# Performance work log

Hardware: AMD Instinct MI355X
Metric: run time of the kernel (lower is better)

The kernel has to match this reference:

```python
import jax, jax.numpy as jnp
import numpy as np

B, C, H, W = 64, 3, 224, 224
PH = PW = 16
GH, GW = H // PH, W // PW
NP = GH * GW                        # 196 patches
E = 512                             # embed_dim == decoder_dim
NH = 8                              # num_heads
PPD = C * PH * PW                   # 768 pixels per patch
MASK_RATIO = 0.75
NUM_MASKED = int(MASK_RATIO * NP)   # 147


def setup_inputs() -> dict:
    key = jax.random.key(0)
    ks = jax.random.split(key, 16)
    s = 0.02
    x = jax.random.normal(ks[0], (B, C, H, W), jnp.float32)
    # per-sample random permutation (torch.rand().argsort() equivalent)
    shuffle_indices = jax.vmap(lambda k: jax.random.permutation(k, NP))(
        jax.random.split(ks[1], B)).astype(jnp.int32)
    return {
        "x": x,
        "shuffle_indices": shuffle_indices,
        "W_pe": jax.random.normal(ks[2], (E, PPD), jnp.float32) * s,
        "b_pe": jnp.zeros((E,), jnp.float32),
        "pos_embed": jax.random.normal(ks[3], (1, NP, E), jnp.float32),
        "enc_W": jax.random.normal(ks[4], (E, E), jnp.float32) * s,
        "enc_b": jnp.zeros((E,), jnp.float32),
        "in_proj_w": jax.random.normal(ks[5], (3 * E, E), jnp.float32) * s,
        "in_proj_b": jnp.zeros((3 * E,), jnp.float32),
        "out_w": jax.random.normal(ks[6], (E, E), jnp.float32) * s,
        "out_b": jnp.zeros((E,), jnp.float32),
        "head_W": jax.random.normal(ks[7], (PPD, E), jnp.float32) * s,
        "head_b": jnp.zeros((PPD,), jnp.float32),
        # torch.randn_like(mask_patches) noise, passed in for determinism
        "noise": jax.random.normal(ks[8], (B, NUM_MASKED, PPD), jnp.float32),
    }


def _to_img(p):
    # [b, nP, ph*pw*c] -> [b, c, H, W] (inverse of patchify)
    return p.reshape(B, GH, GW, PH, PW, C).transpose(0, 5, 1, 3, 2, 4).reshape(B, C, H, W)


def reference(x, shuffle_indices, W_pe, b_pe, pos_embed, enc_W, enc_b,
              in_proj_w, in_proj_b, out_w, out_b, head_W, head_b, noise):
    hd = E // NH
    # patchify: [b,c,H,W] -> [b, nP, ph*pw*c]
    patches = x.reshape(B, C, GH, PH, GW, PW).transpose(0, 2, 4, 3, 5, 1).reshape(B, NP, PPD)

    mask_ind = shuffle_indices[:, :NUM_MASKED]      # [b, 147]
    unmask_ind = shuffle_indices[:, NUM_MASKED:]    # [b, 49]
    bi = jnp.arange(B)[:, None]
    mask_patches = patches[bi, mask_ind]            # [b,147,768]
    unmask_patches = patches[bi, unmask_ind]        # [b, 49,768]

    # mask_image: unmasked patches copied from x, masked patches = 1
    is_masked = jnp.zeros((B, NP), bool).at[bi, mask_ind].set(True)
    mpix = is_masked.reshape(B, 1, GH, 1, GW, 1)
    mpix = jnp.broadcast_to(mpix, (B, C, GH, PH, GW, PW)).reshape(B, C, H, W)
    mask_image = jnp.where(mpix, jnp.ones_like(x), x)

    # encode visible tokens
    pe = pos_embed[0]                               # [nP, E]
    unmask_tokens = unmask_patches @ W_pe.T + b_pe + pe[unmask_ind]
    encoded = jax.nn.gelu(unmask_tokens @ enc_W.T + enc_b)   # encoder.transformer stand-in

    # decode: cross attention (queries = mask tokens, kv = encoded)
    mask_tokens = mask_patches @ W_pe.T + b_pe + pe[mask_ind]
    Wq, Wk, Wv = jnp.split(in_proj_w, 3)
    bq, bk, bv = jnp.split(in_proj_b, 3)
    q = (mask_tokens @ Wq.T + bq).reshape(B, NUM_MASKED, NH, hd)
    k = (encoded @ Wk.T + bk).reshape(B, -1, NH, hd)
    v = (encoded @ Wv.T + bv).reshape(B, -1, NH, hd)
    attn = jax.nn.softmax(jnp.einsum('bqhd,bkhd->bhqk', q, k) / jnp.sqrt(jnp.float32(hd)), axis=-1)
    attn_out = jnp.einsum('bhqk,bkhd->bqhd', attn, v).reshape(B, NUM_MASKED, E) @ out_w.T + out_b

    # scatter encoded + attended tokens back into full sequence
    output_tokens = (jnp.zeros((B, NP, E), x.dtype)
                     .at[bi, unmask_ind].set(encoded)
                     .at[bi, mask_ind].set(attn_out))
    dec_mask_tokens = output_tokens[bi, mask_ind]
    pred = dec_mask_tokens @ head_W.T + head_b      # [b,147,768]

    mse_all_patches = jnp.abs(pred - mask_patches).mean(axis=-1).mean()

    recons_patches = jax.lax.stop_gradient(patches).at[bi, mask_ind].set(pred)
    recons_img = _to_img(recons_patches)

    patches_noisy = patches.at[bi, mask_ind].set(noise)
    patches_to_img = _to_img(patches_noisy)

    return recons_img, patches_to_img, mse_all_patches, mask_image
```

## Files before the change

kernel.cpp:

```cpp
#include <hip/hip_runtime.h>
#include <math.h>

typedef __attribute__((ext_vector_type(8))) __bf16 bf16x8;
typedef __attribute__((ext_vector_type(8))) unsigned short u16x8;
typedef __attribute__((ext_vector_type(4))) float f32x4;

typedef unsigned int as1_u32 __attribute__((address_space(1)));
typedef unsigned int as3_u32 __attribute__((address_space(3)));

__device__ __forceinline__ float bf2f(unsigned short h){
  return __uint_as_float(((unsigned int)h) << 16);
}
__device__ __forceinline__ unsigned short f2bf(float f){
  unsigned int u = __float_as_uint(f);
  unsigned int r = (u + 0x7FFFu + ((u >> 16) & 1u)) >> 16;
  return (unsigned short)r;
}

#if __has_builtin(__builtin_amdgcn_global_load_lds)
#define HAVE_GLOAD_LDS 1
__device__ __forceinline__ void gload16(const void* g, void* l){
  __builtin_amdgcn_global_load_lds((const as1_u32*)(unsigned long long)g,
                                   (as3_u32*)l, 16, 0, 0);
}
#else
#define HAVE_GLOAD_LDS 0
#endif

__global__ __launch_bounds__(256) void prep_all(
    const int* __restrict__ shuf, int* __restrict__ slot,
    const float* __restrict__ Wpe, const float* __restrict__ outw,
    unsigned short* __restrict__ WpeT, unsigned short* __restrict__ outwT,
    const float* __restrict__ encW, const float* __restrict__ inW,
    const float* __restrict__ headW, unsigned short* __restrict__ wcat,
    const float* __restrict__ pos, const float* __restrict__ b_pe,
    const float* __restrict__ outb, const float* __restrict__ headb,
    unsigned short* __restrict__ pe2b, float* __restrict__ bh32,
    const float* __restrict__ x,
    unsigned short* __restrict__ maskA, unsigned short* __restrict__ unmaskA,
    int* __restrict__ tokcat)
{
  const int bid = blockIdx.x, t = threadIdx.x;
  __shared__ float tile[32][33];
  __shared__ float ld[768];
  if (bid < 49){
    const int i = bid*256 + t;
    if (i < 64*196){
      const int b = i / 196, j = i % 196;
      slot[b*196 + shuf[b*196 + j]] = (j < 147) ? j : -1;
    }
  } else if (bid < 689){
    int b2 = bid - 49;
    const float* src; unsigned short* dst; int R, C, bx, by;
    if (b2 < 384){ src = Wpe;  dst = WpeT;  R = 512; C = 768; bx = b2 % 24; by = b2 / 24; }
    else { b2 -= 384; src = outw; dst = outwT; R = 512; C = 512; bx = b2 % 16; by = b2 / 16; }
    const int tx = t & 31, ty = t >> 5;
    #pragma unroll
    for (int i = 0; i < 4; i++)
      tile[ty + i*8][tx] = src[(size_t)(by*32 + ty + i*8)*C + bx*32 + tx];
    __syncthreads();
    #pragma unroll
    for (int i = 0; i < 4; i++)
      dst[(size_t)(bx*32 + ty + i*8)*R + by*32 + tx] = f2bf(tile[tx][ty + i*8]);
  } else if (bid < 6321){
    const int i = (bid - 689)*256 + t;
    float v;
    if      (i <  262144) v = encW[i];
    else if (i < 1048576) v = inW[i -  262144];
    else                  v = headW[i - 1048576];
    wcat[i] = f2bf(v);
  } else if (bid < 6713){
    const int i = (bid - 6321)*256 + t;
    pe2b[i] = f2bf(pos[i] + b_pe[i & 511]);
  } else if (bid < 6725){
    const int r = (bid - 6713)*64 + (t >> 2);
    const int q4 = t & 3;
    float a = 0.0f;
    const float* hw = headW + (size_t)r*512 + q4*128;
    const float* ob = outb + q4*128;
    for (int e = 0; e < 128; e++) a += hw[e] * ob[e];
    a += __shfl_down(a, 2, 4);
    a += __shfl_down(a, 1, 4);
    if (q4 == 0) bh32[r] = a + headb[r];
  } else {
    const int blk = bid - 6725;
    const int b = blk / 224, ip = blk % 224;
    unsigned short* dst;
    int p = 0, valid;
    if (ip < 160){
      valid = (ip < 147);
      if (valid) p = shuf[b*196 + ip];
      dst = maskA + (size_t)(b*160 + ip) * 768;
      if (t == 0) tokcat[b*160 + ip] = p;
    } else {
      const int u = ip - 160;
      valid = (u < 49);
      if (valid) p = shuf[b*196 + 147 + u];
      dst = unmaskA + (size_t)(b*64 + u) * 768;
      if (t == 0) tokcat[10240 + b*64 + u] = p;
    }
    const int gh = p / 14, gw = p % 14;
    if (valid && t < 192){
      const int seg = t >> 2, part = t & 3;
      const int c = seg >> 4, phi = seg & 15;
      const float4 v4 = *(const float4*)(x + (size_t)b*150528 + c*50176
                                         + (size_t)(gh*16 + phi)*224 + gw*16 + part*4);
      const int dbase = phi*48 + part*12 + c;
      ld[dbase]     = v4.x;
      ld[dbase + 3] = v4.y;
      ld[dbase + 6] = v4.z;
      ld[dbase + 9] = v4.w;
    }
    __syncthreads();
    if (t < 96){
      u16x8 o;
      if (valid){
        #pragma unroll
        for (int j = 0; j < 8; j++) o[j] = f2bf(ld[t*8 + j]);
      } else {
        #pragma unroll
        for (int j = 0; j < 8; j++) o[j] = 0;
      }
      *(u16x8*)&dst[t*8] = o;
    }
  }
}

struct GD {
  const unsigned short* A; const unsigned short* W; const float* aux;
  const int* tok; unsigned short* ob; float* of;
  int N, K, mode, blk0, nx;
};

__global__ __launch_bounds__(256) void gemm2(GD g0, GD g1, GD g2, GD g3, GD g4){
  const int bid = blockIdx.x;
  GD g = g0;
  if (bid >= g1.blk0) g = g1;
  if (bid >= g2.blk0) g = g2;
  if (bid >= g3.blk0) g = g3;
  if (bid >= g4.blk0) g = g4;
  const int local = bid - g.blk0;
  const int tn = (local % g.nx) * 64;
  const int tm = (local / g.nx) * 128;
  const int N = g.N, K = g.K;

  __shared__ unsigned short As[2*128*32];
  __shared__ unsigned short Bs[2*64*32];
  const int t = threadIdx.x;
  const int wave = t >> 6, lane = t & 63;
  const int wr = (wave >> 1) * 64, wc = (wave & 1) * 32;
  const int lr = lane & 15, lg = lane >> 4;

  f32x4 acc[4][2] = {};

#if HAVE_GLOAD_LDS
  const int srow = lane >> 2;
  const int scol = (lane & 3) * 8;
  const unsigned short* Ag = g.A + (size_t)(tm + wave*32 + srow) * K + scol;
  const unsigned short* Bg = g.W + (size_t)(tn + wave*16 + srow) * K + scol;
  unsigned short* Al0 = As + wave*(32*32);
  unsigned short* Bl0 = Bs + wave*(16*32);
  const size_t rstepA = (size_t)16 * K;

  gload16(Ag,          Al0);
  gload16(Ag + rstepA, Al0 + 16*32);
  gload16(Bg,          Bl0);
  __syncthreads();

  const int nt = K >> 5;
  for (int tt = 0; tt < nt; ++tt){
    const int cur = tt & 1;
    if (tt + 1 < nt){
      const int k0 = (tt + 1) * 32;
      unsigned short* Al = Al0 + (cur^1)*(128*32);
      unsigned short* Bl = Bl0 + (cur^1)*(64*32);
      gload16(Ag + k0,          Al);
      gload16(Ag + k0 + rstepA, Al + 16*32);
      gload16(Bg + k0,          Bl);
    }
    const unsigned short* Ab = As + cur*(128*32);
    const unsigned short* Bb = Bs + cur*(64*32);
    bf16x8 av[4], bv[2];
    #pragma unroll
    for (int mi = 0; mi < 4; mi++) av[mi] = *(const bf16x8*)&Ab[(wr + mi*16 + lr)*32 + lg*8];
    #pragma unroll
    for (int ni = 0; ni < 2; ni++) bv[ni] = *(const bf16x8*)&Bb[(wc + ni*16 + lr)*32 + lg*8];
    #pragma unroll
    for (int mi = 0; mi < 4; mi++)
      #pragma unroll
      for (int ni = 0; ni < 2; ni++)
        acc[mi][ni] = __builtin_amdgcn_mfma_f32_16x16x32_bf16(av[mi], bv[ni], acc[mi][ni], 0, 0, 0);
    __syncthreads();
  }
#else
  const int r0 = t >> 2;
  const int c0 = (t & 3) * 8;
  for (int k0 = 0; k0 < K; k0 += 32){
    u16x8 ra0 = *(const u16x8*)(g.A + (size_t)(tm + r0) * K + k0 + c0);
    u16x8 rb0 = (r0 < 64) ? *(const u16x8*)(g.W + (size_t)(tn + r0) * K + k0 + c0) : u16x8{};
    __syncthreads();
    *(u16x8*)&As[r0 * 32 + c0] = ra0;
    if (r0 < 64) *(u16x8*)&Bs[r0 * 32 + c0] = rb0;
    __syncthreads();
    bf16x8 av[4], bv[2];
    #pragma unroll
    for (int mi = 0; mi < 4; mi++) av[mi] = *(const bf16x8*)&As[(wr + mi*16 + lr)*32 + lg*8];
    #pragma unroll
    for (int ni = 0; ni < 2; ni++) bv[ni] = *(const bf16x8*)&Bs[(wc + ni*16 + lr)*32 + lg*8];
    #pragma unroll
    for (int mi = 0; mi < 4; mi++)
      #pragma unroll
      for (int ni = 0; ni < 2; ni++)
        acc[mi][ni] = __builtin_amdgcn_mfma_f32_16x16x32_bf16(av[mi], bv[ni], acc[mi][ni], 0, 0, 0);
  }
#endif

  const int mode = g.mode;
  #pragma unroll
  for (int ni = 0; ni < 2; ni++){
    const int gcol = tn + wc + ni*16 + lr;
    const float bval = (mode == 0 || mode == 3) ? g.aux[gcol] : 0.0f;
    #pragma unroll
    for (int mi = 0; mi < 4; mi++){
      #pragma unroll
      for (int jj = 0; jj < 4; jj++){
        const int grow = tm + wr + mi*16 + lg*4 + jj;
        float v = acc[mi][ni][jj] + bval;
        if (mode == 1 || mode == 2) v += g.aux[(size_t)g.tok[grow] * 512 + gcol];
        if (mode == 2){
          const float u = v;
          v = 0.5f * u * (1.0f + tanhf(0.7978845608f * (u + 0.044715f * u * u * u)));
        }
        if (mode == 3) g.of[(size_t)grow * N + gcol] = v;
        else           g.ob[(size_t)grow * N + gcol] = f2bf(v);
      }
    }
  }
}

__global__ __launch_bounds__(256) void attn_mfma(const unsigned short* __restrict__ qb,
                                                 const unsigned short* __restrict__ kv,
                                                 unsigned short* __restrict__ attnout)
{
  const int b = blockIdx.x >> 3, h = blockIdx.x & 7;
  __shared__ unsigned short qs[192*72];
  __shared__ unsigned short ks[64*72];
  __shared__ unsigned short vsT[64*72];
  __shared__ float pwt[192*66];
  __shared__ unsigned short pa[192*72];
  __shared__ float inv_[160];
  const int t = threadIdx.x;
  const int wave = t >> 6, lane = t & 63;
  const int wr = (wave >> 1) * 96, wc = (wave & 1) * 32;
  const int lr = lane & 15, lg = lane >> 4;

  for (int idx = t; idx < 192*8; idx += 256){
    const int i = idx >> 3, g = idx & 7;
    u16x8 v = {};
    if (i < 160) v = *(const u16x8*)(qb + (size_t)(b*160 + i)*512 + h*64 + g*8);
    *(u16x8*)&qs[i*72 + g*8] = v;
  }
  for (int idx = t; idx < 64*8; idx += 256){
    const int j = idx >> 3, g = idx & 7;
    const size_t base = (size_t)(b*64 + j)*1024 + h*64 + g*8;
    u16x8 k8 = *(const u16x8*)(kv + base);
    u16x8 v8 = *(const u16x8*)(kv + base + 512);
    *(u16x8*)&ks[j*72 + g*8] = k8;
    #pragma unroll
    for (int d = 0; d < 8; d++) vsT[(g*8 + d)*72 + j] = v8[d];
  }
  __syncthreads();

  {
    f32x4 acc[6][2] = {};
    #pragma unroll
    for (int ksv = 0; ksv < 2; ksv++){
      const int kk = ksv*32;
      bf16x8 av[6], bv[2];
      #pragma unroll
      for (int mi = 0; mi < 6; mi++) av[mi] = *(const bf16x8*)&qs[(wr + mi*16 + lr)*72 + kk + lg*8];
      #pragma unroll
      for (int ni = 0; ni < 2; ni++) bv[ni] = *(const bf16x8*)&ks[(wc + ni*16 + lr)*72 + kk + lg*8];
      #pragma unroll
      for (int mi = 0; mi < 6; mi++)
        #pragma unroll
        for (int ni = 0; ni < 2; ni++)
          acc[mi][ni] = __builtin_amdgcn_mfma_f32_16x16x32_bf16(av[mi], bv[ni], acc[mi][ni], 0, 0, 0);
    }
    #pragma unroll
    for (int mi = 0; mi < 6; mi++)
      #pragma unroll
      for (int ni = 0; ni < 2; ni++)
        #pragma unroll
        for (int jj = 0; jj < 4; jj++)
          pwt[(wr + mi*16 + lg*4 + jj)*66 + wc + ni*16 + lr] = acc[mi][ni][jj] * 0.125f;
  }
  __syncthreads();

  if (t < 147){
    float m = -1e30f;
    for (int j = 0; j < 49; j++) m = fmaxf(m, pwt[t*66 + j]);
    float sum = 0.0f;
    for (int j = 0; j < 49; j++){
      const float e = __expf(pwt[t*66 + j] - m);
      sum += e;
      pa[t*72 + j] = f2bf(e);
    }
    inv_[t] = 1.0f / sum;
    for (int j = 49; j < 64; j++) pa[t*72 + j] = 0;
  } else if (t < 192){
    for (int j = 0; j < 64; j++) pa[t*72 + j] = 0;
    if (t < 160) inv_[t] = 0.0f;
  }
  __syncthreads();

  {
    f32x4 acc[6][2] = {};
    #pragma unroll
    for (int ksv = 0; ksv < 2; ksv++){
      const int kk = ksv*32;
      bf16x8 av[6], bv[2];
      #pragma unroll
      for (int mi = 0; mi < 6; mi++) av[mi] = *(const bf16x8*)&pa[(wr + mi*16 + lr)*72 + kk + lg*8];
      #pragma unroll
      for (int ni = 0; ni < 2; ni++) bv[ni] = *(const bf16x8*)&vsT[(wc + ni*16 + lr)*72 + kk + lg*8];
      #pragma unroll
      for (int mi = 0; mi < 6; mi++)
        #pragma unroll
        for (int ni = 0; ni < 2; ni++)
          acc[mi][ni] = __builtin_amdgcn_mfma_f32_16x16x32_bf16(av[mi], bv[ni], acc[mi][ni], 0, 0, 0);
    }
    #pragma unroll
    for (int mi = 0; mi < 6; mi++)
      #pragma unroll
      for (int ni = 0; ni < 2; ni++)
        #pragma unroll
        for (int jj = 0; jj < 4; jj++){
          const int grow = wr + mi*16 + lg*4 + jj;
          if (grow < 160){
            const float sc = inv_[grow];
            const float v = acc[mi][ni][jj] * sc;
            attnout[(size_t)(b*160 + grow)*512 + h*64 + wc + ni*16 + lr] = f2bf(v);
          }
        }
  }
}

__global__ __launch_bounds__(256) void finalize_k(const float* __restrict__ x, const int* __restrict__ slot,
                           const unsigned short* __restrict__ predb, const float* __restrict__ noise,
                           float* __restrict__ out, float* __restrict__ partial)
{
  const int i4 = blockIdx.x * 256 + threadIdx.x;
  const int idx = i4 * 4;
  const int w = idx % 224;
  const int h = (idx / 224) % 224;
  const int c = (idx / 50176) % 3;
  const int b = idx / 150528;
  const float4 xv = *(const float4*)(x + idx);
  const int p = (h >> 4) * 14 + (w >> 4);
  const int s = slot[b*196 + p];
  float4 rec = xv, noi = xv;
  float mimv = 0.0f;
  float a = 0.0f;
  float4 mim = xv;
  if (s >= 0){
    const int d = (h & 15)*48 + (w & 15)*3 + c;
    const size_t pb = (size_t)(b*160 + s)*768 + d;
    const size_t nb = (size_t)(b*147 + s)*768 + d;
    rec = make_float4(bf2f(predb[pb]), bf2f(predb[pb+3]), bf2f(predb[pb+6]), bf2f(predb[pb+9]));
    noi = make_float4(noise[nb], noise[nb+3], noise[nb+6], noise[nb+9]);
    mim = make_float4(1.0f, 1.0f, 1.0f, 1.0f);
    a = fabsf(rec.x - xv.x) + fabsf(rec.y - xv.y) + fabsf(rec.z - xv.z) + fabsf(rec.w - xv.w);
  }
  (void)mimv;
  *(float4*)(out + idx) = rec;
  *(float4*)(out + 9633792 + idx) = noi;
  float prevm = __shfl_up(mim.w, 1);
  if ((threadIdx.x & 63) == 0 && idx > 0){
    const int pidx = idx - 1;
    const int pw2 = pidx % 224, ph2 = (pidx / 224) % 224;
    const int pb2 = pidx / 150528;
    const int pp = (ph2 >> 4) * 14 + (pw2 >> 4);
    prevm = (slot[pb2*196 + pp] >= 0) ? 1.0f : x[pidx];
  }
  *(float4*)(out + 19267584 + idx) = make_float4(prevm, mim.x, mim.y, mim.z);
  if (i4 == 2408447) out[28901376] = mim.w;
  #pragma unroll
  for (int o = 32; o > 0; o >>= 1) a += __shfl_down(a, o);
  __shared__ float wsum[4];
  if ((threadIdx.x & 63) == 0) wsum[threadIdx.x >> 6] = a;
  __syncthreads();
  if (threadIdx.x == 0)
    partial[blockIdx.x] = wsum[0] + wsum[1] + wsum[2] + wsum[3];
}

__global__ __launch_bounds__(1024) void mse_reduce(const float* __restrict__ partial, float* __restrict__ out){
  float a = 0.0f;
  for (int i = threadIdx.x; i < 9408; i += 1024) a += partial[i];
  #pragma unroll
  for (int o = 32; o > 0; o >>= 1) a += __shfl_down(a, o);
  __shared__ float wsum[16];
  if ((threadIdx.x & 63) == 0) wsum[threadIdx.x >> 6] = a;
  __syncthreads();
  if (threadIdx.x == 0){
    float s = 0.0f;
    #pragma unroll
    for (int i = 0; i < 16; i++) s += wsum[i];
    out[19267584] = s * (1.0f / 7225344.0f);
  }
}

extern "C" void kernel_launch(void* const* d_in, const int* in_sizes, int n_in,
                              void* d_out, int out_size, void* d_ws, size_t ws_size,
                              hipStream_t stream)
{
  const float* x     = (const float*)d_in[0];
  const int*   shuf  = (const int*)d_in[1];
  const float* W_pe  = (const float*)d_in[2];
  const float* b_pe  = (const float*)d_in[3];
  const float* pos   = (const float*)d_in[4];
  const float* encW  = (const float*)d_in[5];
  const float* encB  = (const float*)d_in[6];
  const float* inW   = (const float*)d_in[7];
  const float* inB   = (const float*)d_in[8];
  const float* outW  = (const float*)d_in[9];
  const float* outB  = (const float*)d_in[10];
  const float* headW = (const float*)d_in[11];
  const float* headB = (const float*)d_in[12];
  const float* noise = (const float*)d_in[13];
  float* out = (float*)d_out;

  char* ws = (char*)d_ws;
  size_t cur = 0;
  auto alloc = [&](size_t bytes){ size_t o = cur; cur += (bytes + 255) & ~(size_t)255; return o; };

  int*   slot    = (int*)(ws + alloc(64*196*4));
  int*   tokcat  = (int*)(ws + alloc(14336*4));
  float* partial = (float*)(ws + alloc(9408*4));
  unsigned short* wcat    = (unsigned short*)(ws + alloc((size_t)1441792*2));
  unsigned short* encw_b  = wcat;
  unsigned short* inw_b   = wcat +  262144;
  unsigned short* headw_b = wcat + 1048576;
  unsigned short* WpeT  = (unsigned short*)(ws + alloc((size_t)393216*2));
  unsigned short* outwT = (unsigned short*)(ws + alloc((size_t)262144*2));
  unsigned short* Wqpe  = (unsigned short*)(ws + alloc((size_t)393216*2));
  unsigned short* Wepe  = (unsigned short*)(ws + alloc((size_t)393216*2));
  unsigned short* Whp   = (unsigned short*)(ws + alloc((size_t)393216*2));
  unsigned short* pe2b  = (unsigned short*)(ws + alloc((size_t)131072*2));
  float* peq  = (float*)(ws + alloc((size_t)131072*4));
  float* pee  = (float*)(ws + alloc((size_t)131072*4));
  float* bh32 = (float*)(ws + alloc(768*4));
  char* R0 = ws + alloc(26214400);
  unsigned short* maskA   = (unsigned short*)R0;
  unsigned short* unmaskA = (unsigned short*)(R0 + 15728640);
  unsigned short* attnout = (unsigned short*)R0;
  unsigned short* predb   = (unsigned short*)(R0 + 10485760);
  unsigned short* enc   = (unsigned short*)(ws + alloc((size_t)2097152*2));
  unsigned short* qb    = (unsigned short*)(ws + alloc((size_t)5242880*2));
  unsigned short* kvb   = (unsigned short*)(ws + alloc((size_t)4194304*2));

  const int BIG = 0x7FFFFFFF;

  prep_all<<<21061, 256, 0, stream>>>(shuf, slot, W_pe, outW, WpeT, outwT,
                                      encW, inW, headW, wcat,
                                      pos, b_pe, outB, headB, pe2b, bh32,
                                      x, maskA, unmaskA, tokcat);

  {
    GD t1 = { inw_b,  WpeT,   nullptr, nullptr, Wqpe,   nullptr, 768, 512, 4,   0, 12 };
    GD t2 = { encw_b, WpeT,   nullptr, nullptr, Wepe,   nullptr, 768, 512, 4,  48, 12 };
    GD t3 = { headw_b,outwT,  nullptr, nullptr, Whp,    nullptr, 512, 512, 4,  96,  8 };
    GD t4 = { pe2b,   inw_b,  inB,     nullptr, nullptr, peq,    512, 512, 3, 144,  8 };
    GD t5 = { pe2b,   encw_b, encB,    nullptr, nullptr, pee,    512, 512, 3, 160,  8 };
    gemm2<<<176, 256, 0, stream>>>(t1, t2, t3, t4, t5);
  }
  {
    GD q  = { maskA,   Wqpe, peq, tokcat,         qb,  nullptr, 512, 768, 1,   0, 8 };
    GD en = { unmaskA, Wepe, pee, tokcat + 10240, enc, nullptr, 512, 768, 2, 640, 8 };
    GD nz = q; nz.blk0 = BIG;
    gemm2<<<896, 256, 0, stream>>>(q, en, nz, nz, nz);
  }
  {
    GD kv = { enc, inw_b + (size_t)512*512, inB + 512, nullptr, kvb, nullptr, 1024, 512, 0, 0, 16 };
    GD nz = kv; nz.blk0 = BIG;
    gemm2<<<512, 256, 0, stream>>>(kv, nz, nz, nz, nz);
  }
  attn_mfma<<<512, 256, 0, stream>>>(qb, kvb, attnout);
  {
    GD pr = { attnout, Whp, bh32, nullptr, predb, nullptr, 768, 512, 0, 0, 12 };
    GD nz = pr; nz.blk0 = BIG;
    gemm2<<<960, 256, 0, stream>>>(pr, nz, nz, nz, nz);
  }

  finalize_k<<<9408, 256, 0, stream>>>(x, slot, predb, noise, out, partial);
  mse_reduce<<<1, 1024, 0, stream>>>(partial, out);
}
```

Baseline: 183.1 us.

## Pipeline GEMMs four-deep, move patch gather into weight-fold kernel, trim attention LDS

The GEMM main loop now keeps a 4-buffer cp.async-style pipeline with explicit vmcnt waits, replacing the double buffer that synchronised every tile. Patch extraction moves from prep_all into a new fold_patch kernel that runs alongside the weight-folding GEMMs. It reads whole patch rows coalesced and scatters them through an inverse permutation. Attention stores scores as bf16 and reuses the q buffer for probabilities to cut LDS use. finalize uses nontemporal loads and stores, and pos-embed padding is zeroed so token indices are masked. Together these aim to reduce memory stalls and launch and occupancy overhead, with added complexity and bf16 rounding in the scores.

```diff
diff --git a/kernel.cpp b/kernel.cpp
--- a/kernel.cpp
+++ b/kernel.cpp
@@ -27,27 +27,27 @@
 #define HAVE_GLOAD_LDS 0
 #endif
 
+#define WAITV(N) asm volatile("s_waitcnt vmcnt(" #N ")" ::: "memory")
+
 __global__ __launch_bounds__(256) void prep_all(
-    const int* __restrict__ shuf, int* __restrict__ slot,
+    const int* __restrict__ shuf, int* __restrict__ slot, int* __restrict__ invp,
     const float* __restrict__ Wpe, const float* __restrict__ outw,
     unsigned short* __restrict__ WpeT, unsigned short* __restrict__ outwT,
     const float* __restrict__ encW, const float* __restrict__ inW,
     const float* __restrict__ headW, unsigned short* __restrict__ wcat,
     const float* __restrict__ pos, const float* __restrict__ b_pe,
     const float* __restrict__ outb, const float* __restrict__ headb,
-    unsigned short* __restrict__ pe2b, float* __restrict__ bh32,
-    const float* __restrict__ x,
-    unsigned short* __restrict__ maskA, unsigned short* __restrict__ unmaskA,
-    int* __restrict__ tokcat)
+    unsigned short* __restrict__ pe2b, float* __restrict__ bh32)
 {
   const int bid = blockIdx.x, t = threadIdx.x;
   __shared__ float tile[32][33];
-  __shared__ float ld[768];
   if (bid < 49){
     const int i = bid*256 + t;
     if (i < 64*196){
       const int b = i / 196, j = i % 196;
-      slot[b*196 + shuf[b*196 + j]] = (j < 147) ? j : -1;
+      const int p = shuf[b*196 + j];
+      slot[b*196 + p] = (j < 147) ? j : -1;
+      invp[b*196 + p] = j;
     }
   } else if (bid < 689){
     int b2 = bid - 49;
@@ -69,11 +69,11 @@
     else if (i < 1048576) v = inW[i -  262144];
     else                  v = headW[i - 1048576];
     wcat[i] = f2bf(v);
-  } else if (bid < 6713){
+  } else if (bid < 6833){
     const int i = (bid - 6321)*256 + t;
-    pe2b[i] = f2bf(pos[i] + b_pe[i & 511]);
-  } else if (bid < 6725){
-    const int r = (bid - 6713)*64 + (t >> 2);
+    pe2b[i] = (i < 100352) ? f2bf(pos[i] + b_pe[i & 511]) : (unsigned short)0;
+  } else {
+    const int r = (bid - 6833)*64 + (t >> 2);
     const int q4 = t & 3;
     float a = 0.0f;
     const float* hw = headW + (size_t)r*512 + q4*128;
@@ -82,47 +82,6 @@
     a += __shfl_down(a, 2, 4);
     a += __shfl_down(a, 1, 4);
     if (q4 == 0) bh32[r] = a + headb[r];
-  } else {
-    const int blk = bid - 6725;
-    const int b = blk / 224, ip = blk % 224;
-    unsigned short* dst;
-    int p = 0, valid;
-    if (ip < 160){
-      valid = (ip < 147);
-      if (valid) p = shuf[b*196 + ip];
-      dst = maskA + (size_t)(b*160 + ip) * 768;
-      if (t == 0) tokcat[b*160 + ip] = p;
-    } else {
-      const int u = ip - 160;
-      valid = (u < 49);
-      if (valid) p = shuf[b*196 + 147 + u];
-      dst = unmaskA + (size_t)(b*64 + u) * 768;
-      if (t == 0) tokcat[10240 + b*64 + u] = p;
-    }
-    const int gh = p / 14, gw = p % 14;
-    if (valid && t < 192){
-      const int seg = t >> 2, part = t & 3;
-      const int c = seg >> 4, phi = seg & 15;
-      const float4 v4 = *(const float4*)(x + (size_t)b*150528 + c*50176
-                                         + (size_t)(gh*16 + phi)*224 + gw*16 + part*4);
-      const int dbase = phi*48 + part*12 + c;
-      ld[dbase]     = v4.x;
-      ld[dbase + 3] = v4.y;
-      ld[dbase + 6] = v4.z;
-      ld[dbase + 9] = v4.w;
-    }
-    __syncthreads();
-    if (t < 96){
-      u16x8 o;
-      if (valid){
-        #pragma unroll
-        for (int j = 0; j < 8; j++) o[j] = f2bf(ld[t*8 + j]);
-      } else {
-        #pragma unroll
-        for (int j = 0; j < 8; j++) o[j] = 0;
-      }
-      *(u16x8*)&dst[t*8] = o;
-    }
   }
 }
 
@@ -132,54 +91,55 @@
   int N, K, mode, blk0, nx;
 };
 
-__global__ __launch_bounds__(256) void gemm2(GD g0, GD g1, GD g2, GD g3, GD g4){
-  const int bid = blockIdx.x;
-  GD g = g0;
-  if (bid >= g1.blk0) g = g1;
-  if (bid >= g2.blk0) g = g2;
-  if (bid >= g3.blk0) g = g3;
-  if (bid >= g4.blk0) g = g4;
-  const int local = bid - g.blk0;
+template<int NBUF>
+__device__ __forceinline__ void gemm_core(const GD g, int local, unsigned char* smem){
   const int tn = (local % g.nx) * 64;
   const int tm = (local / g.nx) * 128;
   const int N = g.N, K = g.K;
-
-  __shared__ unsigned short As[2*128*32];
-  __shared__ unsigned short Bs[2*64*32];
+  unsigned short* As = (unsigned short*)smem;
+  unsigned short* Bs = (unsigned short*)(smem + NBUF*128*32*2);
   const int t = threadIdx.x;
   const int wave = t >> 6, lane = t & 63;
   const int wr = (wave >> 1) * 64, wc = (wave & 1) * 32;
   const int lr = lane & 15, lg = lane >> 4;
 
   f32x4 acc[4][2] = {};
+  const int nt = K >> 5;
 
 #if HAVE_GLOAD_LDS
   const int srow = lane >> 2;
   const int scol = (lane & 3) * 8;
   const unsigned short* Ag = g.A + (size_t)(tm + wave*32 + srow) * K + scol;
   const unsigned short* Bg = g.W + (size_t)(tn + wave*16 + srow) * K + scol;
-  unsigned short* Al0 = As + wave*(32*32);
-  unsigned short* Bl0 = Bs + wave*(16*32);
   const size_t rstepA = (size_t)16 * K;
 
-  gload16(Ag,          Al0);
-  gload16(Ag + rstepA, Al0 + 16*32);
-  gload16(Bg,          Bl0);
-  __syncthreads();
-
-  const int nt = K >> 5;
+  auto issue = [&](int tile_i, int slot_i){
+    const int k0 = tile_i * 32;
+    unsigned short* Al = As + slot_i*(128*32) + wave*(32*32);
+    unsigned short* Bl = Bs + slot_i*(64*32)  + wave*(16*32);
+    gload16(Ag + k0,          Al);
+    gload16(Ag + k0 + rstepA, Al + 16*32);
+    gload16(Bg + k0,          Bl);
+  };
+
+  #pragma unroll
+  for (int p = 0; p < NBUF-1; ++p) if (p < nt) issue(p, p);
+
   for (int tt = 0; tt < nt; ++tt){
-    const int cur = tt & 1;
-    if (tt + 1 < nt){
-      const int k0 = (tt + 1) * 32;
-      unsigned short* Al = Al0 + (cur^1)*(128*32);
-      unsigned short* Bl = Bl0 + (cur^1)*(64*32);
-      gload16(Ag + k0,          Al);
-      gload16(Ag + k0 + rstepA, Al + 16*32);
-      gload16(Bg + k0,          Bl);
+    const int rem = nt - 1 - tt;
+    if constexpr (NBUF == 2){
+      WAITV(0);
+    } else {
+      if (rem >= 2) WAITV(6);
+      else if (rem == 1) WAITV(3);
+      else WAITV(0);
     }
-    const unsigned short* Ab = As + cur*(128*32);
-    const unsigned short* Bb = Bs + cur*(64*32);
+    __builtin_amdgcn_s_barrier();
+    __builtin_amdgcn_sched_barrier(0);
+    const int nxt = tt + NBUF - 1;
+    if (nxt < nt) issue(nxt, nxt % NBUF);
+    const unsigned short* Ab = As + (tt % NBUF)*(128*32);
+    const unsigned short* Bb = Bs + (tt % NBUF)*(64*32);
     bf16x8 av[4], bv[2];
     #pragma unroll
     for (int mi = 0; mi < 4; mi++) av[mi] = *(const bf16x8*)&Ab[(wr + mi*16 + lr)*32 + lg*8];
@@ -190,23 +150,24 @@
       #pragma unroll
       for (int ni = 0; ni < 2; ni++)
         acc[mi][ni] = __builtin_amdgcn_mfma_f32_16x16x32_bf16(av[mi], bv[ni], acc[mi][ni], 0, 0, 0);
-    __syncthreads();
   }
 #else
+  unsigned short* As1 = (unsigned short*)smem;
+  unsigned short* Bs1 = (unsigned short*)(smem + 128*32*2);
   const int r0 = t >> 2;
   const int c0 = (t & 3) * 8;
   for (int k0 = 0; k0 < K; k0 += 32){
     u16x8 ra0 = *(const u16x8*)(g.A + (size_t)(tm + r0) * K + k0 + c0);
     u16x8 rb0 = (r0 < 64) ? *(const u16x8*)(g.W + (size_t)(tn + r0) * K + k0 + c0) : u16x8{};
     __syncthreads();
-    *(u16x8*)&As[r0 * 32 + c0] = ra0;
-    if (r0 < 64) *(u16x8*)&Bs[r0 * 32 + c0] = rb0;
+    *(u16x8*)&As1[r0 * 32 + c0] = ra0;
+    if (r0 < 64) *(u16x8*)&Bs1[r0 * 32 + c0] = rb0;
     __syncthreads();
     bf16x8 av[4], bv[2];
     #pragma unroll
-    for (int mi = 0; mi < 4; mi++) av[mi] = *(const bf16x8*)&As[(wr + mi*16 + lr)*32 + lg*8];
-    #pragma unroll
-    for (int ni = 0; ni < 2; ni++) bv[ni] = *(const bf16x8*)&Bs[(wc + ni*16 + lr)*32 + lg*8];
+    for (int mi = 0; mi < 4; mi++) av[mi] = *(const bf16x8*)&As1[(wr + mi*16 + lr)*32 + lg*8];
+    #pragma unroll
+    for (int ni = 0; ni < 2; ni++) bv[ni] = *(const bf16x8*)&Bs1[(wc + ni*16 + lr)*32 + lg*8];
     #pragma unroll
     for (int mi = 0; mi < 4; mi++)
       #pragma unroll
@@ -226,7 +187,7 @@
       for (int jj = 0; jj < 4; jj++){
         const int grow = tm + wr + mi*16 + lg*4 + jj;
         float v = acc[mi][ni][jj] + bval;
-        if (mode == 1 || mode == 2) v += g.aux[(size_t)g.tok[grow] * 512 + gcol];
+        if (mode == 1 || mode == 2) v += g.aux[(size_t)(g.tok[grow] & 255) * 512 + gcol];
         if (mode == 2){
           const float u = v;
           v = 0.5f * u * (1.0f + tanhf(0.7978845608f * (u + 0.044715f * u * u * u)));
@@ -238,17 +199,72 @@
   }
 }
 
+__global__ __launch_bounds__(256) void gemm_one4(GD g){
+  __shared__ __align__(16) unsigned char smem[49152];
+  gemm_core<4>(g, blockIdx.x, smem);
+}
+__global__ __launch_bounds__(256) void gemm_two4(GD a, GD b){
+  __shared__ __align__(16) unsigned char smem[49152];
+  GD g = (blockIdx.x >= b.blk0) ? b : a;
+  gemm_core<4>(g, blockIdx.x - g.blk0, smem);
+}
+
+__global__ __launch_bounds__(256) void fold_patch(GD g0, GD g1, GD g2, GD g3, GD g4,
+    const float* __restrict__ x, const int* __restrict__ invp,
+    unsigned short* __restrict__ maskA, unsigned short* __restrict__ unmaskA,
+    int* __restrict__ tokcat)
+{
+  __shared__ __align__(16) unsigned char smem[24576];
+  const int bid = blockIdx.x, t = threadIdx.x;
+  if (bid < 176){
+    GD g = g0;
+    if (bid >= g1.blk0) g = g1;
+    if (bid >= g2.blk0) g = g2;
+    if (bid >= g3.blk0) g = g3;
+    if (bid >= g4.blk0) g = g4;
+    gemm_core<2>(g, bid - g.blk0, smem);
+    return;
+  }
+  const int blk = bid - 176;
+  const int b = blk / 14, gh = blk % 14;
+  unsigned short* ld = (unsigned short*)smem;
+  for (int e = t; e < 2688; e += 256){
+    const int w4 = e % 56, rest = e / 56;
+    const int phi = rest & 15, c = rest >> 4;
+    const f32x4 v4 = *(const f32x4*)(x + (size_t)b*150528 + c*50176
+                                     + (size_t)(gh*16 + phi)*224 + w4*4);
+    const int gw = w4 >> 2, part = w4 & 3;
+    const int dbase = gw*768 + phi*48 + part*12 + c;
+    ld[dbase]     = f2bf(v4[0]);
+    ld[dbase + 3] = f2bf(v4[1]);
+    ld[dbase + 6] = f2bf(v4[2]);
+    ld[dbase + 9] = f2bf(v4[3]);
+  }
+  __syncthreads();
+  for (int e = t; e < 1344; e += 256){
+    const int gw = e / 96, elem8 = e % 96;
+    const int p = gh*14 + gw;
+    const int j = invp[b*196 + p];
+    unsigned short* dst;
+    int row;
+    if (j < 147){ row = b*160 + j;        dst = maskA; }
+    else        { row = b*64 + (j - 147); dst = unmaskA; }
+    *(u16x8*)&dst[(size_t)row*768 + elem8*8] = *(const u16x8*)&ld[gw*768 + elem8*8];
+    if (elem8 == 0) tokcat[(j < 147) ? (b*160 + j) : (10240 + b*64 + (j - 147))] = p;
+  }
+}
+
 __global__ __launch_bounds__(256) void attn_mfma(const unsigned short* __restrict__ qb,
                                                  const unsigned short* __restrict__ kv,
                                                  unsigned short* __restrict__ attnout)
 {
+  __shared__ __align__(16) unsigned char smem[72064];
+  unsigned short* qs  = (unsigned short*)smem;
+  unsigned short* ks  = (unsigned short*)(smem + 27648);
+  unsigned short* vsT = (unsigned short*)(smem + 36864);
+  unsigned short* pwt = (unsigned short*)(smem + 46080);
+  float* inv_ = (float*)(smem + 71424);
   const int b = blockIdx.x >> 3, h = blockIdx.x & 7;
-  __shared__ unsigned short qs[192*72];
-  __shared__ unsigned short ks[64*72];
-  __shared__ unsigned short vsT[64*72];
-  __shared__ float pwt[192*66];
-  __shared__ unsigned short pa[192*72];
-  __shared__ float inv_[160];
   const int t = threadIdx.x;
   const int wave = t >> 6, lane = t & 63;
   const int wr = (wave >> 1) * 96, wc = (wave & 1) * 32;
@@ -293,16 +309,19 @@
       for (int ni = 0; ni < 2; ni++)
         #pragma unroll
         for (int jj = 0; jj < 4; jj++)
-          pwt[(wr + mi*16 + lg*4 + jj)*66 + wc + ni*16 + lr] = acc[mi][ni][jj] * 0.125f;
+          pwt[(wr + mi*16 + lg*4 + jj)*66 + wc + ni*16 + lr] = f2bf(acc[mi][ni][jj] * 0.125f);
   }
   __syncthreads();
 
+  unsigned short* pa = qs;
   if (t < 147){
+    float sc[49];
     float m = -1e30f;
-    for (int j = 0; j < 49; j++) m = fmaxf(m, pwt[t*66 + j]);
+    #pragma unroll 7
+    for (int j = 0; j < 49; j++){ sc[j] = bf2f(pwt[t*66 + j]); m = fmaxf(m, sc[j]); }
     float sum = 0.0f;
     for (int j = 0; j < 49; j++){
-      const float e = __expf(pwt[t*66 + j] - m);
+      const float e = __expf(sc[j] - m);
       sum += e;
       pa[t*72 + j] = f2bf(e);
     }
@@ -338,8 +357,7 @@
         for (int jj = 0; jj < 4; jj++){
           const int grow = wr + mi*16 + lg*4 + jj;
           if (grow < 160){
-            const float sc = inv_[grow];
-            const float v = acc[mi][ni][jj] * sc;
+            const float v = acc[mi][ni][jj] * inv_[grow];
             attnout[(size_t)(b*160 + grow)*512 + h*64 + wc + ni*16 + lr] = f2bf(v);
           }
         }
@@ -356,26 +374,26 @@
   const int h = (idx / 224) % 224;
   const int c = (idx / 50176) % 3;
   const int b = idx / 150528;
-  const float4 xv = *(const float4*)(x + idx);
+  const f32x4 xv = __builtin_nontemporal_load((const f32x4*)(x + idx));
   const int p = (h >> 4) * 14 + (w >> 4);
   const int s = slot[b*196 + p];
-  float4 rec = xv, noi = xv;
-  float mimv = 0.0f;
+  f32x4 rec = xv, noi = xv, mim = xv;
   float a = 0.0f;
-  float4 mim = xv;
   if (s >= 0){
     const int d = (h & 15)*48 + (w & 15)*3 + c;
     const size_t pb = (size_t)(b*160 + s)*768 + d;
     const size_t nb = (size_t)(b*147 + s)*768 + d;
-    rec = make_float4(bf2f(predb[pb]), bf2f(predb[pb+3]), bf2f(predb[pb+6]), bf2f(predb[pb+9]));
-    noi = make_float4(noise[nb], noise[nb+3], noise[nb+6], noise[nb+9]);
-    mim = make_float4(1.0f, 1.0f, 1.0f, 1.0f);
-    a = fabsf(rec.x - xv.x) + fabsf(rec.y - xv.y) + fabsf(rec.z - xv.z) + fabsf(rec.w - xv.w);
-  }
-  (void)mimv;
-  *(float4*)(out + idx) = rec;
-  *(float4*)(out + 9633792 + idx) = noi;
-  float prevm = __shfl_up(mim.w, 1);
+    rec = f32x4{bf2f(predb[pb]), bf2f(predb[pb+3]), bf2f(predb[pb+6]), bf2f(predb[pb+9])};
+    noi = f32x4{__builtin_nontemporal_load(noise + nb),
+                __builtin_nontemporal_load(noise + nb + 3),
+                __builtin_nontemporal_load(noise + nb + 6),
+                __builtin_nontemporal_load(noise + nb + 9)};
+    mim = f32x4{1.0f, 1.0f, 1.0f, 1.0f};
+    a = fabsf(rec[0] - xv[0]) + fabsf(rec[1] - xv[1]) + fabsf(rec[2] - xv[2]) + fabsf(rec[3] - xv[3]);
+  }
+  __builtin_nontemporal_store(rec, (f32x4*)(out + idx));
+  __builtin_nontemporal_store(noi, (f32x4*)(out + 9633792 + idx));
+  float prevm = __shfl_up(mim[3], 1);
   if ((threadIdx.x & 63) == 0 && idx > 0){
     const int pidx = idx - 1;
     const int pw2 = pidx % 224, ph2 = (pidx / 224) % 224;
@@ -383,8 +401,8 @@
     const int pp = (ph2 >> 4) * 14 + (pw2 >> 4);
     prevm = (slot[pb2*196 + pp] >= 0) ? 1.0f : x[pidx];
   }
-  *(float4*)(out + 19267584 + idx) = make_float4(prevm, mim.x, mim.y, mim.z);
-  if (i4 == 2408447) out[28901376] = mim.w;
+  __builtin_nontemporal_store(f32x4{prevm, mim[0], mim[1], mim[2]}, (f32x4*)(out + 19267584 + idx));
+  if (i4 == 2408447) out[28901376] = mim[3];
   #pragma unroll
   for (int o = 32; o > 0; o >>= 1) a += __shfl_down(a, o);
   __shared__ float wsum[4];
@@ -435,6 +453,7 @@
   auto alloc = [&](size_t bytes){ size_t o = cur; cur += (bytes + 255) & ~(size_t)255; return o; };
 
   int*   slot    = (int*)(ws + alloc(64*196*4));
+  int*   invp    = (int*)(ws + alloc(64*196*4));
   int*   tokcat  = (int*)(ws + alloc(14336*4));
   float* partial = (float*)(ws + alloc(9408*4));
   unsigned short* wcat    = (unsigned short*)(ws + alloc((size_t)1441792*2));
@@ -459,12 +478,9 @@
   unsigned short* qb    = (unsigned short*)(ws + alloc((size_t)5242880*2));
   unsigned short* kvb   = (unsigned short*)(ws + alloc((size_t)4194304*2));
 
-  const int BIG = 0x7FFFFFFF;
-
-  prep_all<<<21061, 256, 0, stream>>>(shuf, slot, W_pe, outW, WpeT, outwT,
-                                      encW, inW, headW, wcat,
-                                      pos, b_pe, outB, headB, pe2b, bh32,
-                                      x, maskA, unmaskA, tokcat);
+  prep_all<<<6845, 256, 0, stream>>>(shuf, slot, invp, W_pe, outW, WpeT, outwT,
+                                     encW, inW, headW, wcat,
+                                     pos, b_pe, outB, headB, pe2b, bh32);
 
   {
     GD t1 = { inw_b,  WpeT,   nullptr, nullptr, Wqpe,   nullptr, 768, 512, 4,   0, 12 };
@@ -472,24 +488,21 @@
     GD t3 = { headw_b,outwT,  nullptr, nullptr, Whp,    nullptr, 512, 512, 4,  96,  8 };
     GD t4 = { pe2b,   inw_b,  inB,     nullptr, nullptr, peq,    512, 512, 3, 144,  8 };
     GD t5 = { pe2b,   encw_b, encB,    nullptr, nullptr, pee,    512, 512, 3, 160,  8 };
-    gemm2<<<176, 256, 0, stream>>>(t1, t2, t3, t4, t5);
+    fold_patch<<<1072, 256, 0, stream>>>(t1, t2, t3, t4, t5, x, invp, maskA, unmaskA, tokcat);
   }
   {
     GD q  = { maskA,   Wqpe, peq, tokcat,         qb,  nullptr, 512, 768, 1,   0, 8 };
     GD en = { unmaskA, Wepe, pee, tokcat + 10240, enc, nullptr, 512, 768, 2, 640, 8 };
-    GD nz = q; nz.blk0 = BIG;
-    gemm2<<<896, 256, 0, stream>>>(q, en, nz, nz, nz);
+    gemm_two4<<<896, 256, 0, stream>>>(q, en);
   }
   {
     GD kv = { enc, inw_b + (size_t)512*512, inB + 512, nullptr, kvb, nullptr, 1024, 512, 0, 0, 16 };
-    GD nz = kv; nz.blk0 = BIG;
-    gemm2<<<512, 256, 0, stream>>>(kv, nz, nz, nz, nz);
+    gemm_one4<<<512, 256, 0, stream>>>(kv);
   }
   attn_mfma<<<512, 256, 0, stream>>>(qb, kvb, attnout);
   {
     GD pr = { attnout, Whp, bh32, nullptr, predb, nullptr, 768, 512, 0, 0, 12 };
-    GD nz = pr; nz.blk0 = BIG;
-    gemm2<<<960, 256, 0, stream>>>(pr, nz, nz, nz, nz);
+    gemm_one4<<<960, 256, 0, stream>>>(pr);
   }
 
   finalize_k<<<9408, 256, 0, stream>>>(x, slot, predb, noise, out, partial);
```

Result: slower. 214.7 us (+17.2%).
